# Kernel optimization log

Hardware: AMD Instinct MI355X
Metric: run time of the kernel (lower is better)

Reference implementation:

```python
import jax, jax.numpy as jnp
import numpy as np

MODEL_DIM = 4096
NH = 32          # query heads
NG = 8           # kv heads (query groups)
HD = MODEL_DIM // NH   # 128, == kv_head_dim in the module
KV_DIM = NG * HD       # 1024
BASE = 50000.0
B, S = 1, 2048


def setup_inputs() -> dict:
    key = jax.random.key(0)
    ks = jax.random.split(key, 3)
    s = 0.02
    return {
        "x": jax.random.normal(ks[0], (B, S, MODEL_DIM), jnp.float32),
        "Wqkv": jax.random.normal(ks[1], (MODEL_DIM, MODEL_DIM + 2 * KV_DIM), jnp.float32) * s,
        "bqkv": jnp.zeros((MODEL_DIM + 2 * KV_DIM,), jnp.float32),
        "Wo": jax.random.normal(ks[2], (MODEL_DIM, MODEL_DIM), jnp.float32) * s,
        "bo": jnp.zeros((MODEL_DIM,), jnp.float32),
    }


def _rope_tables(seq_len):
    # Llama-style RoPE: inv_freq over even dims, emb = concat(freqs, freqs)
    inv_freq = 1.0 / (BASE ** (jnp.arange(0, HD, 2, dtype=jnp.float32) / HD))
    t = jnp.arange(seq_len, dtype=jnp.float32)  # offset = 0 (no cache)
    freqs = t[:, None] * inv_freq[None, :]      # [S, HD/2]
    emb = jnp.concatenate([freqs, freqs], axis=-1)  # [S, HD]
    return jnp.cos(emb), jnp.sin(emb)


def _rotate_half(x):
    x1, x2 = jnp.split(x, 2, axis=-1)
    return jnp.concatenate([-x2, x1], axis=-1)


def reference(x, Wqkv, bqkv, Wo, bo):
    Bsz, Sl, _ = x.shape
    fused = x @ Wqkv + bqkv                                   # [B, S, D + 2*KV]
    q, k, v = jnp.split(fused, [MODEL_DIM, MODEL_DIM + KV_DIM], axis=-1)
    q = q.reshape(Bsz, Sl, NH, HD).transpose(0, 2, 1, 3)      # [B, NH, S, HD]
    k = k.reshape(Bsz, Sl, NG, HD).transpose(0, 2, 1, 3)      # [B, NG, S, HD]
    v = v.reshape(Bsz, Sl, NG, HD).transpose(0, 2, 1, 3)

    cos, sin = _rope_tables(Sl)                               # [S, HD] each
    q = q * cos + _rotate_half(q) * sin
    k = k * cos + _rotate_half(k) * sin

    # GQA without duplicating KV: group query heads per shared KV head
    G = NH // NG
    qg = q.reshape(Bsz, NG, G, Sl, HD)                        # [B, NG, G, S, HD]
    scale = 1.0 / jnp.sqrt(jnp.asarray(HD, q.dtype))
    scores = jnp.einsum('bngsd,bntd->bngst', qg, k) * scale   # [B, NG, G, S, S]
    causal = jnp.tril(jnp.ones((Sl, Sl), dtype=bool))
    scores = jnp.where(causal, scores, jnp.finfo(scores.dtype).min)
    attn = jax.nn.softmax(scores, axis=-1)
    out = jnp.einsum('bngst,bntd->bngsd', attn, v)            # [B, NG, G, S, HD]
    out = out.reshape(Bsz, NH, Sl, HD).transpose(0, 2, 1, 3).reshape(Bsz, Sl, MODEL_DIM)
    return out @ Wo + bo
```

## Files before the change

kernel.cpp:

```cpp
#include <hip/hip_runtime.h>
#include <hip/hip_bf16.h>
#include <math.h>

#define S_LEN  2048
#define MDIM   4096
#define NHEADS 32
#define NKV    8
#define HD     128
#define KVDIM  1024
#define NFUSED (MDIM + 2 * KVDIM)

typedef short bf16x8 __attribute__((ext_vector_type(8)));
typedef float f32x4 __attribute__((ext_vector_type(4)));

__device__ __forceinline__ unsigned short f2b(float f) {
  union { float f; unsigned int u; } v; v.f = f;
  unsigned int r = v.u + 0x7FFFu + ((v.u >> 16) & 1u);
  return (unsigned short)(r >> 16);
}
__device__ __forceinline__ float b2f(unsigned short h) {
  union { unsigned int u; float f; } v; v.u = ((unsigned int)h) << 16;
  return v.f;
}

__device__ __forceinline__ void async_copy16(const void* g, void* l) {
  __builtin_amdgcn_global_load_lds(
      (const __attribute__((address_space(1))) unsigned int*)g,
      (__attribute__((address_space(3))) unsigned int*)l, 16, 0, 0);
}

__global__ __launch_bounds__(256) void convert_x(
    const float* __restrict__ src, unsigned short* __restrict__ dst) {
  size_t i = (size_t)blockIdx.x * 256 + threadIdx.x;
  const float4 a = ((const float4*)src)[2 * i];
  const float4 b = ((const float4*)src)[2 * i + 1];
  unsigned short o[8] = {f2b(a.x), f2b(a.y), f2b(a.z), f2b(a.w),
                         f2b(b.x), f2b(b.y), f2b(b.z), f2b(b.w)};
  *(int4*)(dst + 8 * i) = *(const int4*)o;
}

__global__ __launch_bounds__(256) void transpose_convert(
    const float* __restrict__ W, unsigned short* __restrict__ WT, int K,
    int N) {
  __shared__ unsigned short t[64 * 72];
  const int k0 = blockIdx.y << 6, n0 = blockIdx.x << 6;
  const int tid = threadIdx.x;
#pragma unroll
  for (int it = 0; it < 4; ++it) {
    int idx = it * 256 + tid;
    int r = idx & 63;
    int c = ((idx >> 6) & 15) << 2;
    const float4 v = *(const float4*)(W + (size_t)(k0 + r) * N + n0 + c);
    t[(c + 0) * 72 + r] = f2b(v.x);
    t[(c + 1) * 72 + r] = f2b(v.y);
    t[(c + 2) * 72 + r] = f2b(v.z);
    t[(c + 3) * 72 + r] = f2b(v.w);
  }
  __syncthreads();
  const int n = tid >> 2, kk = (tid & 3) << 4;
  *(int4*)(WT + (size_t)(n0 + n) * K + k0 + kk) = *(int4*)&t[n * 72 + kk];
  *(int4*)(WT + (size_t)(n0 + n) * K + k0 + kk + 8) =
      *(int4*)&t[n * 72 + kk + 8];
}

__global__ __launch_bounds__(512, 2) void gemm1_kernel(
    const unsigned short* __restrict__ xb,
    const unsigned short* __restrict__ WT, const float* __restrict__ bias,
    unsigned short* __restrict__ Qb, unsigned short* __restrict__ Kb,
    unsigned short* __restrict__ Vt) {
  __shared__ unsigned short sm[2][32768];

  const int tid = threadIdx.x;
  const int bn = blockIdx.x, bm = blockIdx.y;
  const int lane = tid & 63, wave = tid >> 6;
  const int lrow = lane & 15, quad = lane >> 4;
  const int wrow = wave >> 2, wcol = wave & 3;

  f32x4 acc[8][4];
#pragma unroll
  for (int i = 0; i < 8; ++i)
#pragma unroll
    for (int j = 0; j < 4; ++j) {
      f32x4 z = {0.f, 0.f, 0.f, 0.f};
      acc[i][j] = z;
    }

  const int lr8 = lane >> 3, lc8 = lane & 7;
  const int baser = wave * 8 + lr8;
  const size_t swz = (size_t)((lc8 ^ (baser & 7)) << 3);
  const unsigned short* sA = xb + (size_t)(bm * 256 + baser) * MDIM + swz;
  const unsigned short* sB = WT + (size_t)(bn * 256 + baser) * MDIM + swz;

  auto stageA2 = [&](int slot, int k0, int c0) {
#pragma unroll
    for (int c = c0; c < c0 + 2; ++c)
      async_copy16(sA + (size_t)c * 64 * MDIM + k0,
                   &sm[slot][(c * 64 + wave * 8) * 64]);
  };
  auto stageB2 = [&](int slot, int k0, int c0) {
#pragma unroll
    for (int c = c0; c < c0 + 2; ++c)
      async_copy16(sB + (size_t)c * 64 * MDIM + k0,
                   &sm[slot][16384 + (c * 64 + wave * 8) * 64]);
  };

  const int arow = wrow * 128 + lrow;
  const int brow = wcol * 64 + lrow;
  const int co0 = (quad ^ (lrow & 7)) << 3;
  const int co1 = ((4 + quad) ^ (lrow & 7)) << 3;

  stageA2(0, 0, 0);
  stageA2(0, 0, 2);
  stageB2(0, 0, 0);
  stageB2(0, 0, 2);

#pragma unroll 1
  for (int kt = 0; kt < 64; ++kt) {
    const int p = kt & 1;
    asm volatile("s_waitcnt vmcnt(0)" ::: "memory");
    __builtin_amdgcn_s_barrier();
    __builtin_amdgcn_sched_barrier(0);

    const unsigned short* Asl = &sm[p][0];
    const unsigned short* Bsl = &sm[p][16384];
    const int kn0 = (kt + 1) << 6;
    const bool pref = kt < 63;
    bf16x8 bfr[4], af[4];

#pragma unroll
    for (int j = 0; j < 4; ++j)
      bfr[j] = *(const bf16x8*)&Bsl[(brow + j * 16) * 64 + co0];
#pragma unroll
    for (int i = 0; i < 4; ++i)
      af[i] = *(const bf16x8*)&Asl[(arow + i * 16) * 64 + co0];
    if (pref) stageA2(p ^ 1, kn0, 0);
    __builtin_amdgcn_s_barrier();
    asm volatile("s_waitcnt lgkmcnt(0)" ::: "memory");
    __builtin_amdgcn_sched_barrier(0);
    __builtin_amdgcn_s_setprio(1);
#pragma unroll
    for (int i = 0; i < 4; ++i)
#pragma unroll
      for (int j = 0; j < 4; ++j)
        acc[i][j] = __builtin_amdgcn_mfma_f32_16x16x32_bf16(af[i], bfr[j],
                                                            acc[i][j], 0, 0, 0);
    __builtin_amdgcn_s_setprio(0);
    __builtin_amdgcn_s_barrier();

#pragma unroll
    for (int i = 0; i < 4; ++i)
      af[i] = *(const bf16x8*)&Asl[(arow + (4 + i) * 16) * 64 + co0];
    if (pref) stageA2(p ^ 1, kn0, 2);
    __builtin_amdgcn_s_barrier();
    asm volatile("s_waitcnt lgkmcnt(0)" ::: "memory");
    __builtin_amdgcn_sched_barrier(0);
    __builtin_amdgcn_s_setprio(1);
#pragma unroll
    for (int i = 0; i < 4; ++i)
#pragma unroll
      for (int j = 0; j < 4; ++j)
        acc[4 + i][j] = __builtin_amdgcn_mfma_f32_16x16x32_bf16(
            af[i], bfr[j], acc[4 + i][j], 0, 0, 0);
    __builtin_amdgcn_s_setprio(0);
    __builtin_amdgcn_s_barrier();

#pragma unroll
    for (int j = 0; j < 4; ++j)
      bfr[j] = *(const bf16x8*)&Bsl[(brow + j * 16) * 64 + co1];
#pragma unroll
    for (int i = 0; i < 4; ++i)
      af[i] = *(const bf16x8*)&Asl[(arow + i * 16) * 64 + co1];
    if (pref) stageB2(p ^ 1, kn0, 0);
    __builtin_amdgcn_s_barrier();
    asm volatile("s_waitcnt lgkmcnt(0)" ::: "memory");
    __builtin_amdgcn_sched_barrier(0);
    __builtin_amdgcn_s_setprio(1);
#pragma unroll
    for (int i = 0; i < 4; ++i)
#pragma unroll
      for (int j = 0; j < 4; ++j)
        acc[i][j] = __builtin_amdgcn_mfma_f32_16x16x32_bf16(af[i], bfr[j],
                                                            acc[i][j], 0, 0, 0);
    __builtin_amdgcn_s_setprio(0);
    __builtin_amdgcn_s_barrier();

#pragma unroll
    for (int i = 0; i < 4; ++i)
      af[i] = *(const bf16x8*)&Asl[(arow + (4 + i) * 16) * 64 + co1];
    if (pref) stageB2(p ^ 1, kn0, 2);
    __builtin_amdgcn_s_barrier();
    asm volatile("s_waitcnt lgkmcnt(0)" ::: "memory");
    __builtin_amdgcn_sched_barrier(0);
    __builtin_amdgcn_s_setprio(1);
#pragma unroll
    for (int i = 0; i < 4; ++i)
#pragma unroll
      for (int j = 0; j < 4; ++j)
        acc[4 + i][j] = __builtin_amdgcn_mfma_f32_16x16x32_bf16(
            af[i], bfr[j], acc[4 + i][j], 0, 0, 0);
    __builtin_amdgcn_s_setprio(0);
  }
  __syncthreads();

  unsigned short* Ct = &sm[0][0];
#pragma unroll 1
  for (int h = 0; h < 2; ++h) {
    const int slot = 2 * bn + h;
    if ((wcol >> 1) == h) {
#pragma unroll
      for (int i = 0; i < 8; ++i)
#pragma unroll
        for (int j = 0; j < 4; ++j) {
          int lc = (wcol & 1) * 64 + j * 16 + lrow;
          float bv = bias[slot * 128 + lc];
#pragma unroll
          for (int r = 0; r < 4; ++r) {
            int lrw = wrow * 128 + i * 16 + quad * 4 + r;
            Ct[lrw * 132 + lc] = f2b(acc[i][j][r] + bv);
          }
        }
    }
    __syncthreads();

    if (slot < 40) {
#pragma unroll 4
      for (int it = 0; it < 32; ++it) {
        int row = it * 8 + wave;
        int d = lane;
        float x1 = b2f(Ct[row * 132 + d]);
        float x2 = b2f(Ct[row * 132 + d + 64]);
        int s = bm * 256 + row;
        float inv_freq = __expf(-0.16905903569f * (float)d);
        float ang = (float)s * inv_freq;
        float c = cosf(ang), sn = sinf(ang);
        float o1 = x1 * c - x2 * sn;
        float o2 = x2 * c + x1 * sn;
        unsigned short* dst;
        if (slot < 32)
          dst = Qb + ((size_t)slot * S_LEN + s) * HD;
        else
          dst = Kb + ((size_t)(slot - 32) * S_LEN + s) * HD;
        dst[d] = f2b(o1);
        dst[d + 64] = f2b(o2);
      }
    } else {
      const int g = slot - 40;
      unsigned short* Vtg = Vt + (size_t)g * HD * S_LEN;
      const int dp = tid >> 3;
      const int sq = (tid & 7) << 5;
      unsigned short buf0[32], buf1[32];
#pragma unroll
      for (int i = 0; i < 32; ++i) {
        unsigned int w = *(const unsigned int*)&Ct[(sq + i) * 132 + 2 * dp];
        buf0[i] = (unsigned short)(w & 0xffffu);
        buf1[i] = (unsigned short)(w >> 16);
      }
      const int s0 = bm * 256 + sq;
#pragma unroll
      for (int c = 0; c < 2; ++c) {
        unsigned short* dst = Vtg + (size_t)(2 * dp + c) * S_LEN + s0;
        const unsigned short* b = c ? buf1 : buf0;
#pragma unroll
        for (int q4 = 0; q4 < 4; ++q4)
          *(int4*)(dst + q4 * 8) = *(const int4*)(b + q4 * 8);
      }
    }
    __syncthreads();
  }
}

__global__ __launch_bounds__(512, 2) void gemm2_kernel(
    const unsigned short* __restrict__ Ab16,
    const unsigned short* __restrict__ BT, const float* __restrict__ bias,
    float* __restrict__ C) {
  __shared__ unsigned short sm[2][24576];

  const int tid = threadIdx.x;
  const int bn = blockIdx.x, bm = blockIdx.y;
  const int lane = tid & 63, wave = tid >> 6;
  const int lrow = lane & 15, quad = lane >> 4;
  const int wrow = wave >> 2, wcol = wave & 3;

  f32x4 acc[4][4];
#pragma unroll
  for (int i = 0; i < 4; ++i)
#pragma unroll
    for (int j = 0; j < 4; ++j) {
      f32x4 z = {0.f, 0.f, 0.f, 0.f};
      acc[i][j] = z;
    }

  const int lr8 = lane >> 3, lc8 = lane & 7;
  const int baser = wave * 8 + lr8;
  const size_t swz = (size_t)((lc8 ^ (baser & 7)) << 3);
  const unsigned short* sA = Ab16 + (size_t)(bm * 128 + baser) * MDIM + swz;
  const unsigned short* sB = BT + (size_t)(bn * 256 + baser) * MDIM + swz;

  auto stageA2 = [&](int slot, int k0) {
#pragma unroll
    for (int c = 0; c < 2; ++c)
      async_copy16(sA + (size_t)c * 64 * MDIM + k0,
                   &sm[slot][(c * 64 + wave * 8) * 64]);
  };
  auto stageB1 = [&](int slot, int k0, int c) {
    async_copy16(sB + (size_t)c * 64 * MDIM + k0,
                 &sm[slot][8192 + (c * 64 + wave * 8) * 64]);
  };

  const int arow = wrow * 64 + lrow;
  const int brow = wcol * 64 + lrow;
  const int co0 = (quad ^ (lrow & 7)) << 3;
  const int co1 = ((4 + quad) ^ (lrow & 7)) << 3;

  stageA2(0, 0);
  stageB1(0, 0, 0);
  stageB1(0, 0, 1);
  stageB1(0, 0, 2);
  stageB1(0, 0, 3);

#pragma unroll 1
  for (int kt = 0; kt < 64; ++kt) {
    const int p = kt & 1;
    asm volatile("s_waitcnt vmcnt(0)" ::: "memory");
    __builtin_amdgcn_s_barrier();
    __builtin_amdgcn_sched_barrier(0);

    const unsigned short* Asl = &sm[p][0];
    const unsigned short* Bsl = &sm[p][8192];
    const int kn0 = (kt + 1) << 6;
    const bool pref = kt < 63;
    bf16x8 bfr[4], af[4];

#pragma unroll
    for (int j = 0; j < 4; ++j)
      bfr[j] = *(const bf16x8*)&Bsl[(brow + j * 16) * 64 + co0];
#pragma unroll
    for (int i = 0; i < 4; ++i)
      af[i] = *(const bf16x8*)&Asl[(arow + i * 16) * 64 + co0];
    if (pref) {
      stageA2(p ^ 1, kn0);
      stageB1(p ^ 1, kn0, 0);
    }
    __builtin_amdgcn_s_barrier();
    asm volatile("s_waitcnt lgkmcnt(0)" ::: "memory");
    __builtin_amdgcn_sched_barrier(0);
    __builtin_amdgcn_s_setprio(1);
#pragma unroll
    for (int i = 0; i < 4; ++i)
#pragma unroll
      for (int j = 0; j < 4; ++j)
        acc[i][j] = __builtin_amdgcn_mfma_f32_16x16x32_bf16(af[i], bfr[j],
                                                            acc[i][j], 0, 0, 0);
    __builtin_amdgcn_s_setprio(0);
    __builtin_amdgcn_s_barrier();

#pragma unroll
    for (int j = 0; j < 4; ++j)
      bfr[j] = *(const bf16x8*)&Bsl[(brow + j * 16) * 64 + co1];
#pragma unroll
    for (int i = 0; i < 4; ++i)
      af[i] = *(const bf16x8*)&Asl[(arow + i * 16) * 64 + co1];
    if (pref) {
      stageB1(p ^ 1, kn0, 1);
      stageB1(p ^ 1, kn0, 2);
      stageB1(p ^ 1, kn0, 3);
    }
    __builtin_amdgcn_s_barrier();
    asm volatile("s_waitcnt lgkmcnt(0)" ::: "memory");
    __builtin_amdgcn_sched_barrier(0);
    __builtin_amdgcn_s_setprio(1);
#pragma unroll
    for (int i = 0; i < 4; ++i)
#pragma unroll
      for (int j = 0; j < 4; ++j)
        acc[i][j] = __builtin_amdgcn_mfma_f32_16x16x32_bf16(af[i], bfr[j],
                                                            acc[i][j], 0, 0, 0);
    __builtin_amdgcn_s_setprio(0);
  }

#pragma unroll
  for (int i = 0; i < 4; ++i)
#pragma unroll
    for (int j = 0; j < 4; ++j) {
      int gcol = bn * 256 + wcol * 64 + j * 16 + lrow;
      float bv = bias[gcol];
#pragma unroll
      for (int r = 0; r < 4; ++r) {
        int grow = bm * 128 + wrow * 64 + i * 16 + quad * 4 + r;
        C[(size_t)grow * MDIM + gcol] = acc[i][j][r] + bv;
      }
    }
}

__device__ __forceinline__ void stage_kv(const unsigned short* __restrict__ Kg,
                                         const unsigned short* __restrict__ Vg,
                                         int jtile, unsigned short* KsBuf,
                                         unsigned short* VsBuf, int wv,
                                         int lane) {
  const unsigned short* kg = Kg + (size_t)jtile * 64 * HD;
  const unsigned short* vg = Vg + jtile * 64;
#pragma unroll
  for (int it = 0; it < 4; ++it) {
    int kr = wv * 16 + it * 4 + (lane >> 4);
    async_copy16(kg + (size_t)kr * HD + (((lane & 15) ^ (kr & 7)) << 3),
                 KsBuf + (wv * 16 + it * 4) * 128);
    int vr = wv * 32 + it * 8 + (lane >> 3);
    async_copy16(vg + (size_t)vr * S_LEN + (((lane & 7) ^ (vr & 7)) << 3),
                 VsBuf + (wv * 32 + it * 8) * 64);
  }
}

__global__ __launch_bounds__(256, 2) void flash_kernel(
    const unsigned short* __restrict__ Qb, const unsigned short* __restrict__ Kb,
    const unsigned short* __restrict__ Vt, unsigned short* __restrict__ attnb) {
  __shared__ __align__(16) unsigned short Ks[2][64 * 128];
  __shared__ __align__(16) unsigned short Vs[2][128 * 64];
  __shared__ __align__(16) unsigned short Ps[64 * 72];

  const int tid = threadIdx.x;
  const int bid = blockIdx.x;
  const int h = bid & 31;
  const int qt = 31 - (bid >> 5);
  const int g = h >> 2;
  const int wv = tid >> 6, lane = tid & 63;
  const int lrow = lane & 15, quad = lane >> 4;
  const float scale = 0.08838834764831845f;

  const unsigned short* Qg = Qb + ((size_t)h * S_LEN + qt * 64) * HD;
  bf16x8 qf[4];
#pragma unroll
  for (int ks = 0; ks < 4; ++ks)
    qf[ks] = *(const bf16x8*)(Qg + (size_t)(wv * 16 + lrow) * HD + ks * 32 +
                              quad * 8);

  bf16x8 ones;
#pragma unroll
  for (int i = 0; i < 8; ++i) ones[i] = (short)0x3F80;

  const unsigned short* Kg = Kb + (size_t)g * S_LEN * HD;
  const unsigned short* Vg = Vt + (size_t)g * HD * S_LEN;

  f32x4 l_acc = {0.f, 0.f, 0.f, 0.f};
  f32x4 o_acc[8];
#pragma unroll
  for (int jc = 0; jc < 8; ++jc) {
    f32x4 z = {0.f, 0.f, 0.f, 0.f};
    o_acc[jc] = z;
  }

  stage_kv(Kg, Vg, 0, &Ks[0][0], &Vs[0][0], wv, lane);

  for (int jt = 0; jt <= qt; ++jt) {
    const int cb = jt & 1;
    asm volatile("s_waitcnt vmcnt(0)" ::: "memory");
    __builtin_amdgcn_s_barrier();
    __builtin_amdgcn_sched_barrier(0);

    if (jt < qt)
      stage_kv(Kg, Vg, jt + 1, &Ks[cb ^ 1][0], &Vs[cb ^ 1][0], wv, lane);

    f32x4 s_acc[4];
#pragma unroll
    for (int j = 0; j < 4; ++j) {
      f32x4 z = {0.f, 0.f, 0.f, 0.f};
      s_acc[j] = z;
    }
#pragma unroll
    for (int ks = 0; ks < 4; ++ks)
#pragma unroll
      for (int j = 0; j < 4; ++j) {
        int row = j * 16 + lrow;
        bf16x8 bk = *(const bf16x8*)&Ks[cb][row * 128 +
                                           (((ks * 4 + quad) ^ (row & 7)) << 3)];
        s_acc[j] = __builtin_amdgcn_mfma_f32_16x16x32_bf16(qf[ks], bk,
                                                           s_acc[j], 0, 0, 0);
      }

    if (jt == qt) {
#pragma unroll
      for (int r = 0; r < 4; ++r) {
        int grow = qt * 64 + wv * 16 + quad * 4 + r;
#pragma unroll
        for (int j = 0; j < 4; ++j) {
          int gcol = jt * 64 + j * 16 + lrow;
          float p =
              (gcol <= grow) ? __expf(s_acc[j][r] * scale - 12.0f) : 0.f;
          Ps[(wv * 16 + quad * 4 + r) * 72 + j * 16 + lrow] = f2b(p);
        }
      }
    } else {
#pragma unroll
      for (int r = 0; r < 4; ++r)
#pragma unroll
        for (int j = 0; j < 4; ++j) {
          float p = __expf(s_acc[j][r] * scale - 12.0f);
          Ps[(wv * 16 + quad * 4 + r) * 72 + j * 16 + lrow] = f2b(p);
        }
    }
    asm volatile("s_waitcnt lgkmcnt(0)" ::: "memory");
    __builtin_amdgcn_sched_barrier(0);

#pragma unroll
    for (int kk = 0; kk < 2; ++kk) {
      bf16x8 ap =
          *(const bf16x8*)&Ps[(wv * 16 + lrow) * 72 + kk * 32 + 8 * quad];
      l_acc = __builtin_amdgcn_mfma_f32_16x16x32_bf16(ap, ones, l_acc, 0, 0, 0);
#pragma unroll
      for (int jc = 0; jc < 8; ++jc) {
        int row = jc * 16 + lrow;
        bf16x8 bv = *(const bf16x8*)&Vs[cb][row * 64 +
                                            (((kk * 4 + quad) ^ (row & 7)) << 3)];
        o_acc[jc] = __builtin_amdgcn_mfma_f32_16x16x32_bf16(ap, bv, o_acc[jc],
                                                            0, 0, 0);
      }
    }
    __builtin_amdgcn_s_barrier();
  }

#pragma unroll
  for (int r = 0; r < 4; ++r) {
    float inv_l = 1.0f / l_acc[r];
    int row = qt * 64 + wv * 16 + quad * 4 + r;
#pragma unroll
    for (int jc = 0; jc < 8; ++jc) {
      int col = jc * 16 + lrow;
      attnb[(size_t)row * MDIM + h * HD + col] = f2b(o_acc[jc][r] * inv_l);
    }
  }
}

extern "C" void kernel_launch(void* const* d_in, const int* in_sizes, int n_in,
                              void* d_out, int out_size, void* d_ws,
                              size_t ws_size, hipStream_t stream) {
  const float* x = (const float*)d_in[0];
  const float* Wqkv = (const float*)d_in[1];
  const float* bqkv = (const float*)d_in[2];
  const float* Wo = (const float*)d_in[3];
  const float* bo = (const float*)d_in[4];
  float* out = (float*)d_out;

  unsigned char* ws = (unsigned char*)d_ws;
  unsigned short* WT = (unsigned short*)ws;
  unsigned short* WoT = (unsigned short*)ws;
  unsigned short* attnb = (unsigned short*)(ws + 33554432);
  unsigned short* Qb = (unsigned short*)(ws + 50331648);
  unsigned short* Kb = (unsigned short*)(ws + 67108864);
  unsigned short* Vt = (unsigned short*)(ws + 71303168);
  unsigned short* xb = (unsigned short*)d_out;

  convert_x<<<(S_LEN * MDIM / 8) / 256, 256, 0, stream>>>(x, xb);
  transpose_convert<<<dim3(NFUSED / 64, MDIM / 64), 256, 0, stream>>>(
      Wqkv, WT, MDIM, NFUSED);
  gemm1_kernel<<<dim3(NFUSED / 256, S_LEN / 256), 512, 0, stream>>>(
      xb, WT, bqkv, Qb, Kb, Vt);
  transpose_convert<<<dim3(MDIM / 64, MDIM / 64), 256, 0, stream>>>(Wo, WoT,
                                                                    MDIM, MDIM);
  flash_kernel<<<S_LEN / 64 * NHEADS, 256, 0, stream>>>(Qb, Kb, Vt, attnb);
  gemm2_kernel<<<dim3(MDIM / 256, S_LEN / 128), 512, 0, stream>>>(attnb, WoT,
                                                                  bo, out);
}
```

Measured before the change: 500.7 us.

## Reorder GEMM k-loop phases and use partial vmcnt waits for finer prefetch overlap

Result: no change. 495.9 us (-0.9%).

```diff
diff --git a/kernel.cpp b/kernel.cpp
--- a/kernel.cpp
+++ b/kernel.cpp
@@ -91,17 +91,13 @@
   const unsigned short* sA = xb + (size_t)(bm * 256 + baser) * MDIM + swz;
   const unsigned short* sB = WT + (size_t)(bn * 256 + baser) * MDIM + swz;
 
-  auto stageA2 = [&](int slot, int k0, int c0) {
-#pragma unroll
-    for (int c = c0; c < c0 + 2; ++c)
-      async_copy16(sA + (size_t)c * 64 * MDIM + k0,
-                   &sm[slot][(c * 64 + wave * 8) * 64]);
+  auto stageA1 = [&](int slot, int k0, int c) {
+    async_copy16(sA + (size_t)c * 64 * MDIM + k0,
+                 &sm[slot][(c * 64 + wave * 8) * 64]);
   };
-  auto stageB2 = [&](int slot, int k0, int c0) {
-#pragma unroll
-    for (int c = c0; c < c0 + 2; ++c)
-      async_copy16(sB + (size_t)c * 64 * MDIM + k0,
-                   &sm[slot][16384 + (c * 64 + wave * 8) * 64]);
+  auto stageB1 = [&](int slot, int k0, int c) {
+    async_copy16(sB + (size_t)c * 64 * MDIM + k0,
+                 &sm[slot][16384 + (c * 64 + wave * 8) * 64]);
   };
 
   const int arow = wrow * 128 + lrow;
@@ -109,31 +105,38 @@
   const int co0 = (quad ^ (lrow & 7)) << 3;
   const int co1 = ((4 + quad) ^ (lrow & 7)) << 3;
 
-  stageA2(0, 0, 0);
-  stageA2(0, 0, 2);
-  stageB2(0, 0, 0);
-  stageB2(0, 0, 2);
+  stageA1(0, 0, 0);
+  stageA1(0, 0, 2);
+  stageB1(0, 0, 0);
+  stageB1(0, 0, 1);
+  stageB1(0, 0, 2);
+  stageB1(0, 0, 3);
+  stageA1(0, 0, 1);
+  stageA1(0, 0, 3);
 
 #pragma unroll 1
   for (int kt = 0; kt < 64; ++kt) {
     const int p = kt & 1;
-    asm volatile("s_waitcnt vmcnt(0)" ::: "memory");
-    __builtin_amdgcn_s_barrier();
-    __builtin_amdgcn_sched_barrier(0);
-
     const unsigned short* Asl = &sm[p][0];
     const unsigned short* Bsl = &sm[p][16384];
     const int kn0 = (kt + 1) << 6;
     const bool pref = kt < 63;
-    bf16x8 bfr[4], af[4];
+    bf16x8 bfr0[4], bfr1[4], af[4];
+
+    asm volatile("s_waitcnt vmcnt(2)" ::: "memory");
+    __builtin_amdgcn_s_barrier();
+    __builtin_amdgcn_sched_barrier(0);
 
 #pragma unroll
     for (int j = 0; j < 4; ++j)
-      bfr[j] = *(const bf16x8*)&Bsl[(brow + j * 16) * 64 + co0];
+      bfr0[j] = *(const bf16x8*)&Bsl[(brow + j * 16) * 64 + co0];
 #pragma unroll
     for (int i = 0; i < 4; ++i)
       af[i] = *(const bf16x8*)&Asl[(arow + i * 16) * 64 + co0];
-    if (pref) stageA2(p ^ 1, kn0, 0);
+    if (pref) {
+      stageA1(p ^ 1, kn0, 0);
+      stageA1(p ^ 1, kn0, 2);
+    }
     __builtin_amdgcn_s_barrier();
     asm volatile("s_waitcnt lgkmcnt(0)" ::: "memory");
     __builtin_amdgcn_sched_barrier(0);
@@ -142,15 +145,46 @@
     for (int i = 0; i < 4; ++i)
 #pragma unroll
       for (int j = 0; j < 4; ++j)
-        acc[i][j] = __builtin_amdgcn_mfma_f32_16x16x32_bf16(af[i], bfr[j],
+        acc[i][j] = __builtin_amdgcn_mfma_f32_16x16x32_bf16(af[i], bfr0[j],
                                                             acc[i][j], 0, 0, 0);
     __builtin_amdgcn_s_setprio(0);
     __builtin_amdgcn_s_barrier();
 
 #pragma unroll
+    for (int j = 0; j < 4; ++j)
+      bfr1[j] = *(const bf16x8*)&Bsl[(brow + j * 16) * 64 + co1];
+#pragma unroll
+    for (int i = 0; i < 4; ++i)
+      af[i] = *(const bf16x8*)&Asl[(arow + i * 16) * 64 + co1];
+    if (pref) {
+      stageB1(p ^ 1, kn0, 0);
+      stageB1(p ^ 1, kn0, 1);
+    }
+    __builtin_amdgcn_s_barrier();
+    asm volatile("s_waitcnt lgkmcnt(0)" ::: "memory");
+    __builtin_amdgcn_sched_barrier(0);
+    __builtin_amdgcn_s_setprio(1);
+#pragma unroll
+    for (int i = 0; i < 4; ++i)
+#pragma unroll
+      for (int j = 0; j < 4; ++j)
+        acc[i][j] = __builtin_amdgcn_mfma_f32_16x16x32_bf16(af[i], bfr1[j],
+                                                            acc[i][j], 0, 0, 0);
+    __builtin_amdgcn_s_setprio(0);
+    if (pref)
+      asm volatile("s_waitcnt vmcnt(4)" ::: "memory");
+    else
+      asm volatile("s_waitcnt vmcnt(0)" ::: "memory");
+    __builtin_amdgcn_s_barrier();
+    __builtin_amdgcn_sched_barrier(0);
+
+#pragma unroll
     for (int i = 0; i < 4; ++i)
       af[i] = *(const bf16x8*)&Asl[(arow + (4 + i) * 16) * 64 + co0];
-    if (pref) stageA2(p ^ 1, kn0, 2);
+    if (pref) {
+      stageB1(p ^ 1, kn0, 2);
+      stageB1(p ^ 1, kn0, 3);
+    }
     __builtin_amdgcn_s_barrier();
     asm volatile("s_waitcnt lgkmcnt(0)" ::: "memory");
     __builtin_amdgcn_sched_barrier(0);
@@ -160,34 +194,17 @@
 #pragma unroll
       for (int j = 0; j < 4; ++j)
         acc[4 + i][j] = __builtin_amdgcn_mfma_f32_16x16x32_bf16(
-            af[i], bfr[j], acc[4 + i][j], 0, 0, 0);
+            af[i], bfr0[j], acc[4 + i][j], 0, 0, 0);
     __builtin_amdgcn_s_setprio(0);
     __builtin_amdgcn_s_barrier();
 
 #pragma unroll
-    for (int j = 0; j < 4; ++j)
-      bfr[j] = *(const bf16x8*)&Bsl[(brow + j * 16) * 64 + co1];
-#pragma unroll
-    for (int i = 0; i < 4; ++i)
-      af[i] = *(const bf16x8*)&Asl[(arow + i * 16) * 64 + co1];
-    if (pref) stageB2(p ^ 1, kn0, 0);
-    __builtin_amdgcn_s_barrier();
-    asm volatile("s_waitcnt lgkmcnt(0)" ::: "memory");
-    __builtin_amdgcn_sched_barrier(0);
-    __builtin_amdgcn_s_setprio(1);
-#pragma unroll
-    for (int i = 0; i < 4; ++i)
-#pragma unroll
-      for (int j = 0; j < 4; ++j)
-        acc[i][j] = __builtin_amdgcn_mfma_f32_16x16x32_bf16(af[i], bfr[j],
-                                                            acc[i][j], 0, 0, 0);
-    __builtin_amdgcn_s_setprio(0);
-    __builtin_amdgcn_s_barrier();
-
-#pragma unroll
     for (int i = 0; i < 4; ++i)
       af[i] = *(const bf16x8*)&Asl[(arow + (4 + i) * 16) * 64 + co1];
-    if (pref) stageB2(p ^ 1, kn0, 2);
+    if (pref) {
+      stageA1(p ^ 1, kn0, 1);
+      stageA1(p ^ 1, kn0, 3);
+    }
     __builtin_amdgcn_s_barrier();
     asm volatile("s_waitcnt lgkmcnt(0)" ::: "memory");
     __builtin_amdgcn_sched_barrier(0);
@@ -197,7 +214,7 @@
 #pragma unroll
       for (int j = 0; j < 4; ++j)
         acc[4 + i][j] = __builtin_amdgcn_mfma_f32_16x16x32_bf16(
-            af[i], bfr[j], acc[4 + i][j], 0, 0, 0);
+            af[i], bfr1[j], acc[4 + i][j], 0, 0, 0);
     __builtin_amdgcn_s_setprio(0);
   }
   __syncthreads();
```

## Use 4-wave 128x128 warp tiles in QKV GEMM and precompute RoPE table

Applied to the files above, without the earlier changes.

Result: slower. 757.8 us (+51.4%).

```diff
diff --git a/kernel.cpp b/kernel.cpp
--- a/kernel.cpp
+++ b/kernel.cpp
@@ -37,6 +37,14 @@
   unsigned short o[8] = {f2b(a.x), f2b(a.y), f2b(a.z), f2b(a.w),
                          f2b(b.x), f2b(b.y), f2b(b.z), f2b(b.w)};
   *(int4*)(dst + 8 * i) = *(const int4*)o;
+}
+
+__global__ __launch_bounds__(256) void rope_table(float2* __restrict__ rtab) {
+  int t = blockIdx.x * 256 + threadIdx.x;
+  int s = t >> 6, d = t & 63;
+  float inv_freq = __expf(-0.16905903569f * (float)d);
+  float ang = (float)s * inv_freq;
+  rtab[t] = make_float2(cosf(ang), sinf(ang));
 }
 
 __global__ __launch_bounds__(256) void transpose_convert(
@@ -63,56 +71,56 @@
       *(int4*)&t[n * 72 + kk + 8];
 }
 
-__global__ __launch_bounds__(512, 2) void gemm1_kernel(
+__global__ __launch_bounds__(256, 1) void gemm1_kernel(
     const unsigned short* __restrict__ xb,
     const unsigned short* __restrict__ WT, const float* __restrict__ bias,
-    unsigned short* __restrict__ Qb, unsigned short* __restrict__ Kb,
-    unsigned short* __restrict__ Vt) {
+    const float2* __restrict__ rtab, unsigned short* __restrict__ Qb,
+    unsigned short* __restrict__ Kb, unsigned short* __restrict__ Vt) {
   __shared__ unsigned short sm[2][32768];
 
   const int tid = threadIdx.x;
   const int bn = blockIdx.x, bm = blockIdx.y;
   const int lane = tid & 63, wave = tid >> 6;
   const int lrow = lane & 15, quad = lane >> 4;
-  const int wrow = wave >> 2, wcol = wave & 3;
-
-  f32x4 acc[8][4];
+  const int wrow = wave >> 1, wcol = wave & 1;
+
+  f32x4 acc[8][8];
 #pragma unroll
   for (int i = 0; i < 8; ++i)
 #pragma unroll
-    for (int j = 0; j < 4; ++j) {
+    for (int j = 0; j < 8; ++j) {
       f32x4 z = {0.f, 0.f, 0.f, 0.f};
       acc[i][j] = z;
     }
 
-  const int lr8 = lane >> 3, lc8 = lane & 7;
-  const int baser = wave * 8 + lr8;
-  const size_t swz = (size_t)((lc8 ^ (baser & 7)) << 3);
-  const unsigned short* sA = xb + (size_t)(bm * 256 + baser) * MDIM + swz;
-  const unsigned short* sB = WT + (size_t)(bn * 256 + baser) * MDIM + swz;
-
-  auto stageA2 = [&](int slot, int k0, int c0) {
-#pragma unroll
-    for (int c = c0; c < c0 + 2; ++c)
-      async_copy16(sA + (size_t)c * 64 * MDIM + k0,
-                   &sm[slot][(c * 64 + wave * 8) * 64]);
+  const size_t swz = (size_t)(((lane & 7) ^ (lane >> 3)) << 3);
+  const unsigned short* sA =
+      xb + (size_t)(bm * 256 + wave * 64 + (lane >> 3)) * MDIM + swz;
+  const unsigned short* sB =
+      WT + (size_t)(bn * 256 + wave * 64 + (lane >> 3)) * MDIM + swz;
+
+  auto stageA4 = [&](int slot, int k0, int m0) {
+#pragma unroll
+    for (int m = m0; m < m0 + 4; ++m)
+      async_copy16(sA + (size_t)m * 8 * MDIM + k0,
+                   &sm[slot][(wave * 64 + m * 8) * 64]);
   };
-  auto stageB2 = [&](int slot, int k0, int c0) {
-#pragma unroll
-    for (int c = c0; c < c0 + 2; ++c)
-      async_copy16(sB + (size_t)c * 64 * MDIM + k0,
-                   &sm[slot][16384 + (c * 64 + wave * 8) * 64]);
+  auto stageB4 = [&](int slot, int k0, int m0) {
+#pragma unroll
+    for (int m = m0; m < m0 + 4; ++m)
+      async_copy16(sB + (size_t)m * 8 * MDIM + k0,
+                   &sm[slot][16384 + (wave * 64 + m * 8) * 64]);
   };
 
   const int arow = wrow * 128 + lrow;
-  const int brow = wcol * 64 + lrow;
+  const int brow = wcol * 128 + lrow;
   const int co0 = (quad ^ (lrow & 7)) << 3;
   const int co1 = ((4 + quad) ^ (lrow & 7)) << 3;
 
-  stageA2(0, 0, 0);
-  stageA2(0, 0, 2);
-  stageB2(0, 0, 0);
-  stageB2(0, 0, 2);
+  stageA4(0, 0, 0);
+  stageA4(0, 0, 4);
+  stageB4(0, 0, 0);
+  stageB4(0, 0, 4);
 
 #pragma unroll 1
   for (int kt = 0; kt < 64; ++kt) {
@@ -125,79 +133,71 @@
     const unsigned short* Bsl = &sm[p][16384];
     const int kn0 = (kt + 1) << 6;
     const bool pref = kt < 63;
-    bf16x8 bfr[4], af[4];
-
-#pragma unroll
-    for (int j = 0; j < 4; ++j)
-      bfr[j] = *(const bf16x8*)&Bsl[(brow + j * 16) * 64 + co0];
-#pragma unroll
-    for (int i = 0; i < 4; ++i)
-      af[i] = *(const bf16x8*)&Asl[(arow + i * 16) * 64 + co0];
-    if (pref) stageA2(p ^ 1, kn0, 0);
-    __builtin_amdgcn_s_barrier();
-    asm volatile("s_waitcnt lgkmcnt(0)" ::: "memory");
+    bf16x8 b0[8], b1[8], a0[4], a1[4], a2[4], a3[4];
+
+#pragma unroll
+    for (int j = 0; j < 8; ++j)
+      b0[j] = *(const bf16x8*)&Bsl[(brow + j * 16) * 64 + co0];
+#pragma unroll
+    for (int i = 0; i < 4; ++i)
+      a0[i] = *(const bf16x8*)&Asl[(arow + i * 16) * 64 + co0];
+    if (pref) {
+      stageA4(p ^ 1, kn0, 0);
+      stageA4(p ^ 1, kn0, 4);
+    }
+#pragma unroll
+    for (int i = 0; i < 4; ++i)
+      a1[i] = *(const bf16x8*)&Asl[(arow + (4 + i) * 16) * 64 + co0];
+    asm volatile("s_waitcnt lgkmcnt(4)" ::: "memory");
     __builtin_amdgcn_sched_barrier(0);
     __builtin_amdgcn_s_setprio(1);
 #pragma unroll
     for (int i = 0; i < 4; ++i)
 #pragma unroll
-      for (int j = 0; j < 4; ++j)
-        acc[i][j] = __builtin_amdgcn_mfma_f32_16x16x32_bf16(af[i], bfr[j],
+      for (int j = 0; j < 8; ++j)
+        acc[i][j] = __builtin_amdgcn_mfma_f32_16x16x32_bf16(a0[i], b0[j],
                                                             acc[i][j], 0, 0, 0);
     __builtin_amdgcn_s_setprio(0);
-    __builtin_amdgcn_s_barrier();
-
-#pragma unroll
-    for (int i = 0; i < 4; ++i)
-      af[i] = *(const bf16x8*)&Asl[(arow + (4 + i) * 16) * 64 + co0];
-    if (pref) stageA2(p ^ 1, kn0, 2);
-    __builtin_amdgcn_s_barrier();
-    asm volatile("s_waitcnt lgkmcnt(0)" ::: "memory");
+    if (pref) stageB4(p ^ 1, kn0, 0);
+#pragma unroll
+    for (int j = 0; j < 8; ++j)
+      b1[j] = *(const bf16x8*)&Bsl[(brow + j * 16) * 64 + co1];
+#pragma unroll
+    for (int i = 0; i < 4; ++i)
+      a2[i] = *(const bf16x8*)&Asl[(arow + i * 16) * 64 + co1];
+    asm volatile("s_waitcnt lgkmcnt(12)" ::: "memory");
     __builtin_amdgcn_sched_barrier(0);
     __builtin_amdgcn_s_setprio(1);
 #pragma unroll
     for (int i = 0; i < 4; ++i)
 #pragma unroll
-      for (int j = 0; j < 4; ++j)
+      for (int j = 0; j < 8; ++j)
         acc[4 + i][j] = __builtin_amdgcn_mfma_f32_16x16x32_bf16(
-            af[i], bfr[j], acc[4 + i][j], 0, 0, 0);
+            a1[i], b0[j], acc[4 + i][j], 0, 0, 0);
     __builtin_amdgcn_s_setprio(0);
-    __builtin_amdgcn_s_barrier();
-
-#pragma unroll
-    for (int j = 0; j < 4; ++j)
-      bfr[j] = *(const bf16x8*)&Bsl[(brow + j * 16) * 64 + co1];
-#pragma unroll
-    for (int i = 0; i < 4; ++i)
-      af[i] = *(const bf16x8*)&Asl[(arow + i * 16) * 64 + co1];
-    if (pref) stageB2(p ^ 1, kn0, 0);
-    __builtin_amdgcn_s_barrier();
-    asm volatile("s_waitcnt lgkmcnt(0)" ::: "memory");
+    if (pref) stageB4(p ^ 1, kn0, 4);
+#pragma unroll
+    for (int i = 0; i < 4; ++i)
+      a3[i] = *(const bf16x8*)&Asl[(arow + (4 + i) * 16) * 64 + co1];
+    asm volatile("s_waitcnt lgkmcnt(4)" ::: "memory");
     __builtin_amdgcn_sched_barrier(0);
     __builtin_amdgcn_s_setprio(1);
 #pragma unroll
     for (int i = 0; i < 4; ++i)
 #pragma unroll
-      for (int j = 0; j < 4; ++j)
-        acc[i][j] = __builtin_amdgcn_mfma_f32_16x16x32_bf16(af[i], bfr[j],
+      for (int j = 0; j < 8; ++j)
+        acc[i][j] = __builtin_amdgcn_mfma_f32_16x16x32_bf16(a2[i], b1[j],
                                                             acc[i][j], 0, 0, 0);
     __builtin_amdgcn_s_setprio(0);
-    __builtin_amdgcn_s_barrier();
-
-#pragma unroll
-    for (int i = 0; i < 4; ++i)
-      af[i] = *(const bf16x8*)&Asl[(arow + (4 + i) * 16) * 64 + co1];
-    if (pref) stageB2(p ^ 1, kn0, 2);
-    __builtin_amdgcn_s_barrier();
     asm volatile("s_waitcnt lgkmcnt(0)" ::: "memory");
     __builtin_amdgcn_sched_barrier(0);
     __builtin_amdgcn_s_setprio(1);
 #pragma unroll
     for (int i = 0; i < 4; ++i)
 #pragma unroll
-      for (int j = 0; j < 4; ++j)
+      for (int j = 0; j < 8; ++j)
         acc[4 + i][j] = __builtin_amdgcn_mfma_f32_16x16x32_bf16(
-            af[i], bfr[j], acc[4 + i][j], 0, 0, 0);
+            a3[i], b1[j], acc[4 + i][j], 0, 0, 0);
     __builtin_amdgcn_s_setprio(0);
   }
   __syncthreads();
@@ -206,12 +206,12 @@
 #pragma unroll 1
   for (int h = 0; h < 2; ++h) {
     const int slot = 2 * bn + h;
-    if ((wcol >> 1) == h) {
+    if (wcol == h) {
 #pragma unroll
       for (int i = 0; i < 8; ++i)
 #pragma unroll
-        for (int j = 0; j < 4; ++j) {
-          int lc = (wcol & 1) * 64 + j * 16 + lrow;
+        for (int j = 0; j < 8; ++j) {
+          int lc = j * 16 + lrow;
           float bv = bias[slot * 128 + lc];
 #pragma unroll
           for (int r = 0; r < 4; ++r) {
@@ -224,17 +224,15 @@
 
     if (slot < 40) {
 #pragma unroll 4
-      for (int it = 0; it < 32; ++it) {
-        int row = it * 8 + wave;
+      for (int it = 0; it < 64; ++it) {
+        int row = it * 4 + wave;
         int d = lane;
         float x1 = b2f(Ct[row * 132 + d]);
         float x2 = b2f(Ct[row * 132 + d + 64]);
         int s = bm * 256 + row;
-        float inv_freq = __expf(-0.16905903569f * (float)d);
-        float ang = (float)s * inv_freq;
-        float c = cosf(ang), sn = sinf(ang);
-        float o1 = x1 * c - x2 * sn;
-        float o2 = x2 * c + x1 * sn;
+        float2 cs = rtab[s * 64 + d];
+        float o1 = x1 * cs.x - x2 * cs.y;
+        float o2 = x2 * cs.x + x1 * cs.y;
         unsigned short* dst;
         if (slot < 32)
           dst = Qb + ((size_t)slot * S_LEN + s) * HD;
@@ -246,23 +244,27 @@
     } else {
       const int g = slot - 40;
       unsigned short* Vtg = Vt + (size_t)g * HD * S_LEN;
-      const int dp = tid >> 3;
-      const int sq = (tid & 7) << 5;
-      unsigned short buf0[32], buf1[32];
-#pragma unroll
-      for (int i = 0; i < 32; ++i) {
-        unsigned int w = *(const unsigned int*)&Ct[(sq + i) * 132 + 2 * dp];
-        buf0[i] = (unsigned short)(w & 0xffffu);
-        buf1[i] = (unsigned short)(w >> 16);
-      }
-      const int s0 = bm * 256 + sq;
-#pragma unroll
-      for (int c = 0; c < 2; ++c) {
-        unsigned short* dst = Vtg + (size_t)(2 * dp + c) * S_LEN + s0;
-        const unsigned short* b = c ? buf1 : buf0;
-#pragma unroll
-        for (int q4 = 0; q4 < 4; ++q4)
-          *(int4*)(dst + q4 * 8) = *(const int4*)(b + q4 * 8);
+      const int dp = tid >> 2;
+      const int sq = (tid & 3) << 5;
+#pragma unroll 1
+      for (int vc = 0; vc < 2; ++vc) {
+        unsigned short buf0[32], buf1[32];
+#pragma unroll
+        for (int i = 0; i < 32; ++i) {
+          unsigned int w =
+              *(const unsigned int*)&Ct[(vc * 128 + sq + i) * 132 + 2 * dp];
+          buf0[i] = (unsigned short)(w & 0xffffu);
+          buf1[i] = (unsigned short)(w >> 16);
+        }
+        const int s0 = bm * 256 + vc * 128 + sq;
+#pragma unroll
+        for (int c = 0; c < 2; ++c) {
+          unsigned short* dst = Vtg + (size_t)(2 * dp + c) * S_LEN + s0;
+          const unsigned short* b = c ? buf1 : buf0;
+#pragma unroll
+          for (int q4 = 0; q4 < 4; ++q4)
+            *(int4*)(dst + q4 * 8) = *(const int4*)(b + q4 * 8);
+        }
       }
     }
     __syncthreads();
@@ -547,12 +549,14 @@
   unsigned short* Kb = (unsigned short*)(ws + 67108864);
   unsigned short* Vt = (unsigned short*)(ws + 71303168);
   unsigned short* xb = (unsigned short*)d_out;
+  float2* rtab = (float2*)((unsigned char*)d_out + 16777216);
 
   convert_x<<<(S_LEN * MDIM / 8) / 256, 256, 0, stream>>>(x, xb);
+  rope_table<<<(S_LEN * 64) / 256, 256, 0, stream>>>(rtab);
   transpose_convert<<<dim3(NFUSED / 64, MDIM / 64), 256, 0, stream>>>(
       Wqkv, WT, MDIM, NFUSED);
-  gemm1_kernel<<<dim3(NFUSED / 256, S_LEN / 256), 512, 0, stream>>>(
-      xb, WT, bqkv, Qb, Kb, Vt);
+  gemm1_kernel<<<dim3(NFUSED / 256, S_LEN / 256), 256, 0, stream>>>(
+      xb, WT, bqkv, rtab, Qb, Kb, Vt);
   transpose_convert<<<dim3(MDIM / 64, MDIM / 64), 256, 0, stream>>>(Wo, WoT,
                                                                     MDIM, MDIM);
   flash_kernel<<<S_LEN / 64 * NHEADS, 256, 0, stream>>>(Qb, Kb, Vt, attnb);
```

## Simplify gemm1 main loop schedule and precompute RoPE cos/sin table

Applied to the files above, without the earlier changes.

Measured after the change: 487.6 us. -2.6%, faster.

```diff
diff --git a/kernel.cpp b/kernel.cpp
--- a/kernel.cpp
+++ b/kernel.cpp
@@ -37,6 +37,14 @@
   unsigned short o[8] = {f2b(a.x), f2b(a.y), f2b(a.z), f2b(a.w),
                          f2b(b.x), f2b(b.y), f2b(b.z), f2b(b.w)};
   *(int4*)(dst + 8 * i) = *(const int4*)o;
+}
+
+__global__ __launch_bounds__(256) void rope_table(float2* __restrict__ rtab) {
+  int t = blockIdx.x * 256 + threadIdx.x;
+  int s = t >> 6, d = t & 63;
+  float inv_freq = __expf(-0.16905903569f * (float)d);
+  float ang = (float)s * inv_freq;
+  rtab[t] = make_float2(cosf(ang), sinf(ang));
 }
 
 __global__ __launch_bounds__(256) void transpose_convert(
@@ -66,8 +74,8 @@
 __global__ __launch_bounds__(512, 2) void gemm1_kernel(
     const unsigned short* __restrict__ xb,
     const unsigned short* __restrict__ WT, const float* __restrict__ bias,
-    unsigned short* __restrict__ Qb, unsigned short* __restrict__ Kb,
-    unsigned short* __restrict__ Vt) {
+    const float2* __restrict__ rtab, unsigned short* __restrict__ Qb,
+    unsigned short* __restrict__ Kb, unsigned short* __restrict__ Vt) {
   __shared__ unsigned short sm[2][32768];
 
   const int tid = threadIdx.x;
@@ -91,17 +99,14 @@
   const unsigned short* sA = xb + (size_t)(bm * 256 + baser) * MDIM + swz;
   const unsigned short* sB = WT + (size_t)(bn * 256 + baser) * MDIM + swz;
 
-  auto stageA2 = [&](int slot, int k0, int c0) {
-#pragma unroll
-    for (int c = c0; c < c0 + 2; ++c)
-      async_copy16(sA + (size_t)c * 64 * MDIM + k0,
-                   &sm[slot][(c * 64 + wave * 8) * 64]);
-  };
-  auto stageB2 = [&](int slot, int k0, int c0) {
-#pragma unroll
-    for (int c = c0; c < c0 + 2; ++c)
-      async_copy16(sB + (size_t)c * 64 * MDIM + k0,
-                   &sm[slot][16384 + (c * 64 + wave * 8) * 64]);
+  auto stage = [&](int slot, int k0) {
+#pragma unroll
+    for (int c = 0; c < 4; ++c) {
+      unsigned short* dA = &sm[slot][(c * 64 + wave * 8) * 64];
+      unsigned short* dB = &sm[slot][16384 + (c * 64 + wave * 8) * 64];
+      async_copy16(sA + (size_t)c * 64 * MDIM + k0, dA);
+      async_copy16(sB + (size_t)c * 64 * MDIM + k0, dB);
+    }
   };
 
   const int arow = wrow * 128 + lrow;
@@ -109,95 +114,35 @@
   const int co0 = (quad ^ (lrow & 7)) << 3;
   const int co1 = ((4 + quad) ^ (lrow & 7)) << 3;
 
-  stageA2(0, 0, 0);
-  stageA2(0, 0, 2);
-  stageB2(0, 0, 0);
-  stageB2(0, 0, 2);
-
-#pragma unroll 1
+  stage(0, 0);
+
   for (int kt = 0; kt < 64; ++kt) {
     const int p = kt & 1;
     asm volatile("s_waitcnt vmcnt(0)" ::: "memory");
     __builtin_amdgcn_s_barrier();
     __builtin_amdgcn_sched_barrier(0);
 
+    if (kt < 63) stage(p ^ 1, (kt + 1) << 6);
+
     const unsigned short* Asl = &sm[p][0];
     const unsigned short* Bsl = &sm[p][16384];
-    const int kn0 = (kt + 1) << 6;
-    const bool pref = kt < 63;
-    bf16x8 bfr[4], af[4];
-
-#pragma unroll
-    for (int j = 0; j < 4; ++j)
-      bfr[j] = *(const bf16x8*)&Bsl[(brow + j * 16) * 64 + co0];
-#pragma unroll
-    for (int i = 0; i < 4; ++i)
-      af[i] = *(const bf16x8*)&Asl[(arow + i * 16) * 64 + co0];
-    if (pref) stageA2(p ^ 1, kn0, 0);
-    __builtin_amdgcn_s_barrier();
-    asm volatile("s_waitcnt lgkmcnt(0)" ::: "memory");
-    __builtin_amdgcn_sched_barrier(0);
     __builtin_amdgcn_s_setprio(1);
 #pragma unroll
-    for (int i = 0; i < 4; ++i)
+    for (int kk = 0; kk < 2; ++kk) {
+      const int co = kk ? co1 : co0;
+      bf16x8 bfr[4];
 #pragma unroll
       for (int j = 0; j < 4; ++j)
-        acc[i][j] = __builtin_amdgcn_mfma_f32_16x16x32_bf16(af[i], bfr[j],
-                                                            acc[i][j], 0, 0, 0);
-    __builtin_amdgcn_s_setprio(0);
-    __builtin_amdgcn_s_barrier();
-
-#pragma unroll
-    for (int i = 0; i < 4; ++i)
-      af[i] = *(const bf16x8*)&Asl[(arow + (4 + i) * 16) * 64 + co0];
-    if (pref) stageA2(p ^ 1, kn0, 2);
-    __builtin_amdgcn_s_barrier();
-    asm volatile("s_waitcnt lgkmcnt(0)" ::: "memory");
-    __builtin_amdgcn_sched_barrier(0);
-    __builtin_amdgcn_s_setprio(1);
-#pragma unroll
-    for (int i = 0; i < 4; ++i)
-#pragma unroll
-      for (int j = 0; j < 4; ++j)
-        acc[4 + i][j] = __builtin_amdgcn_mfma_f32_16x16x32_bf16(
-            af[i], bfr[j], acc[4 + i][j], 0, 0, 0);
-    __builtin_amdgcn_s_setprio(0);
-    __builtin_amdgcn_s_barrier();
-
-#pragma unroll
-    for (int j = 0; j < 4; ++j)
-      bfr[j] = *(const bf16x8*)&Bsl[(brow + j * 16) * 64 + co1];
-#pragma unroll
-    for (int i = 0; i < 4; ++i)
-      af[i] = *(const bf16x8*)&Asl[(arow + i * 16) * 64 + co1];
-    if (pref) stageB2(p ^ 1, kn0, 0);
-    __builtin_amdgcn_s_barrier();
-    asm volatile("s_waitcnt lgkmcnt(0)" ::: "memory");
-    __builtin_amdgcn_sched_barrier(0);
-    __builtin_amdgcn_s_setprio(1);
-#pragma unroll
-    for (int i = 0; i < 4; ++i)
-#pragma unroll
-      for (int j = 0; j < 4; ++j)
-        acc[i][j] = __builtin_amdgcn_mfma_f32_16x16x32_bf16(af[i], bfr[j],
-                                                            acc[i][j], 0, 0, 0);
-    __builtin_amdgcn_s_setprio(0);
-    __builtin_amdgcn_s_barrier();
-
-#pragma unroll
-    for (int i = 0; i < 4; ++i)
-      af[i] = *(const bf16x8*)&Asl[(arow + (4 + i) * 16) * 64 + co1];
-    if (pref) stageB2(p ^ 1, kn0, 2);
-    __builtin_amdgcn_s_barrier();
-    asm volatile("s_waitcnt lgkmcnt(0)" ::: "memory");
-    __builtin_amdgcn_sched_barrier(0);
-    __builtin_amdgcn_s_setprio(1);
-#pragma unroll
-    for (int i = 0; i < 4; ++i)
-#pragma unroll
-      for (int j = 0; j < 4; ++j)
-        acc[4 + i][j] = __builtin_amdgcn_mfma_f32_16x16x32_bf16(
-            af[i], bfr[j], acc[4 + i][j], 0, 0, 0);
+        bfr[j] = *(const bf16x8*)&Bsl[(brow + j * 16) * 64 + co];
+#pragma unroll
+      for (int i = 0; i < 8; ++i) {
+        bf16x8 af = *(const bf16x8*)&Asl[(arow + i * 16) * 64 + co];
+#pragma unroll
+        for (int j = 0; j < 4; ++j)
+          acc[i][j] = __builtin_amdgcn_mfma_f32_16x16x32_bf16(
+              af, bfr[j], acc[i][j], 0, 0, 0);
+      }
+    }
     __builtin_amdgcn_s_setprio(0);
   }
   __syncthreads();
@@ -230,11 +175,9 @@
         float x1 = b2f(Ct[row * 132 + d]);
         float x2 = b2f(Ct[row * 132 + d + 64]);
         int s = bm * 256 + row;
-        float inv_freq = __expf(-0.16905903569f * (float)d);
-        float ang = (float)s * inv_freq;
-        float c = cosf(ang), sn = sinf(ang);
-        float o1 = x1 * c - x2 * sn;
-        float o2 = x2 * c + x1 * sn;
+        float2 cs = rtab[s * 64 + d];
+        float o1 = x1 * cs.x - x2 * cs.y;
+        float o2 = x2 * cs.x + x1 * cs.y;
         unsigned short* dst;
         if (slot < 32)
           dst = Qb + ((size_t)slot * S_LEN + s) * HD;
@@ -547,12 +490,14 @@
   unsigned short* Kb = (unsigned short*)(ws + 67108864);
   unsigned short* Vt = (unsigned short*)(ws + 71303168);
   unsigned short* xb = (unsigned short*)d_out;
+  float2* rtab = (float2*)((unsigned char*)d_out + 16777216);
 
   convert_x<<<(S_LEN * MDIM / 8) / 256, 256, 0, stream>>>(x, xb);
+  rope_table<<<(S_LEN * 64) / 256, 256, 0, stream>>>(rtab);
   transpose_convert<<<dim3(NFUSED / 64, MDIM / 64), 256, 0, stream>>>(
       Wqkv, WT, MDIM, NFUSED);
   gemm1_kernel<<<dim3(NFUSED / 256, S_LEN / 256), 512, 0, stream>>>(
-      xb, WT, bqkv, Qb, Kb, Vt);
+      xb, WT, bqkv, rtab, Qb, Kb, Vt);
   transpose_convert<<<dim3(MDIM / 64, MDIM / 64), 256, 0, stream>>>(Wo, WoT,
                                                                     MDIM, MDIM);
   flash_kernel<<<S_LEN / 64 * NHEADS, 256, 0, stream>>>(Qb, Kb, Vt, attnb);
```
